# Kernel tuning notes

Hardware: AMD Instinct MI355X
Metric: run time of the kernel (lower is better)

The kernel has to match this reference:

```python
import jax, jax.numpy as jnp
import numpy as np

N = 100_000      # nodes
E = 1_600_000    # edges (avg degree 16)
C_IN, C_H, C_OUT = 32, 64, 64
G = 64           # graphs in batch


def setup_inputs() -> dict:
    key = jax.random.key(0)
    ks = jax.random.split(key, 10)
    x = jax.random.normal(ks[0], (N, C_IN), jnp.float32)
    edge_index = jax.random.randint(ks[1], (2, E), 0, N, dtype=jnp.int64)
    edge_weight = jax.random.uniform(ks[2], (E,), jnp.float32)
    batch = jnp.sort(jax.random.randint(ks[3], (N,), 0, G, dtype=jnp.int64))
    def lin(k, fan_in, fan_out):
        return jax.random.normal(k, (fan_in, fan_out), jnp.float32) / np.float32(np.sqrt(fan_in))
    W1 = lin(ks[4], C_IN, C_H)
    W2 = lin(ks[5], C_H, C_H)
    W3 = lin(ks[6], C_H, C_OUT)
    b1 = jnp.zeros((C_H,), jnp.float32)
    b2 = jnp.zeros((C_H,), jnp.float32)
    b3 = jnp.zeros((C_OUT,), jnp.float32)
    return {"x": x, "edge_weight": edge_weight, "W1": W1, "b1": b1,
            "W2": W2, "b2": b2, "W3": W3, "b3": b3,
            "edge_index": edge_index, "batch": batch}


def _gcn_norm(edge_index, edge_weight, n):
    # PyG GCNConv default: add self-loops (weight 1), symmetric D^-1/2 A D^-1/2 norm.
    loop = jnp.arange(n, dtype=edge_index.dtype)
    src = jnp.concatenate([edge_index[0], loop])
    dst = jnp.concatenate([edge_index[1], loop])
    ew = jnp.concatenate([edge_weight, jnp.ones((n,), edge_weight.dtype)])
    deg = jax.ops.segment_sum(ew, dst, num_segments=n)
    dis = jnp.where(deg > 0, jax.lax.rsqrt(deg), jnp.float32(0))
    norm = dis[src] * ew * dis[dst]
    return src, dst, norm


def _gcn_layer(h, W, b, src, dst, norm, n):
    h = h @ W                                 # [N, out]
    msg = h[src] * norm[:, None]              # gather + scale  [E+N, out]
    agg = jax.ops.segment_sum(msg, dst, num_segments=n)
    return agg + b


def reference(x, edge_weight, W1, b1, W2, b2, W3, b3, edge_index, batch):
    n = x.shape[0]
    src, dst, norm = _gcn_norm(edge_index, edge_weight, n)  # shared across layers
    h = jax.nn.silu(_gcn_layer(x, W1, b1, src, dst, norm, n))
    # Dropout(0.1) is identity in eval mode
    h = jax.nn.silu(_gcn_layer(h, W2, b2, src, dst, norm, n))
    h = jax.nn.silu(_gcn_layer(h, W3, b3, src, dst, norm, n))
    # global_mean_pool over graphs
    sums = jax.ops.segment_sum(h, batch, num_segments=G)
    counts = jax.ops.segment_sum(jnp.ones((n,), h.dtype), batch, num_segments=G)
    return sums / jnp.maximum(counts, 1)[:, None]
```

## Files before the change

kernel.cpp:

```cpp
#include <hip/hip_runtime.h>
#include <hip/hip_fp16.h>
#include <math.h>


#define NB   256
#define PBLK 1024
#define FIXP_SCALE 1048576.0f
#define FIXP_MASK  ((1ULL << 40) - 1)

__device__ __forceinline__ int lower_bound_i(const int* __restrict__ a, int n, int v) {
    int lo = 0, hi = n;
    while (lo < hi) {
        int m = (lo + hi) >> 1;
        if (a[m] < v) lo = m + 1; else hi = m;
    }
    return lo;
}

__global__ __launch_bounds__(256) void k_bhist(const int* __restrict__ dst,
                                               int* __restrict__ hcnt, int e) {
    __shared__ int hist[NB];
    int tid = threadIdx.x, blk = blockIdx.x;
    hist[tid] = 0;
    __syncthreads();
    int chunk = (e + PBLK - 1) / PBLK;
    int lo = blk * chunk, hi = min(e, lo + chunk);
    for (int i = lo + tid; i < hi; i += 256)
        atomicAdd(&hist[dst[i] >> 9], 1);
    __syncthreads();
    hcnt[tid * PBLK + blk] = hist[tid];
}

__global__ __launch_bounds__(256) void k_bscan(int* __restrict__ hcnt,
                                               int* __restrict__ btot) {
    __shared__ int s[256];
    int b = blockIdx.x, tid = threadIdx.x;
    int* row = hcnt + b * PBLK;
    int a0 = row[4 * tid], a1 = row[4 * tid + 1], a2 = row[4 * tid + 2], a3 = row[4 * tid + 3];
    int tsum = a0 + a1 + a2 + a3;
    s[tid] = tsum;
    __syncthreads();
    for (int off = 1; off < 256; off <<= 1) {
        int t = (tid >= off) ? s[tid - off] : 0;
        __syncthreads();
        s[tid] += t;
        __syncthreads();
    }
    int ex = s[tid] - tsum;
    row[4 * tid] = ex;
    row[4 * tid + 1] = ex + a0;
    row[4 * tid + 2] = ex + a0 + a1;
    row[4 * tid + 3] = ex + a0 + a1 + a2;
    if (tid == 255) btot[b] = s[255];
}

__global__ __launch_bounds__(256) void k_bbase(const int* __restrict__ btot,
                                               int* __restrict__ bbase,
                                               int* __restrict__ rowptr, int n, int e) {
    __shared__ int s[256];
    int tid = threadIdx.x;
    int v = btot[tid];
    s[tid] = v;
    __syncthreads();
    for (int off = 1; off < 256; off <<= 1) {
        int t = (tid >= off) ? s[tid - off] : 0;
        __syncthreads();
        s[tid] += t;
        __syncthreads();
    }
    bbase[tid] = s[tid] - v;
    if (tid == 255) bbase[NB] = s[255];
    if (tid == 0) rowptr[n] = e;
}

__global__ __launch_bounds__(256) void k_bpart(const int* __restrict__ src,
                                               const int* __restrict__ dst,
                                               const float* __restrict__ ew,
                                               const int* __restrict__ hcnt,
                                               const int* __restrict__ bbase,
                                               int2* __restrict__ bedge, int e) {
    __shared__ int cur[NB];
    int tid = threadIdx.x, blk = blockIdx.x;
    cur[tid] = bbase[tid] + hcnt[tid * PBLK + blk];
    __syncthreads();
    int chunk = (e + PBLK - 1) / PBLK;
    int lo = blk * chunk, hi = min(e, lo + chunk);
    for (int i = lo + tid; i < hi; i += 256) {
        int d = dst[i];
        int pos = atomicAdd(&cur[d >> 9], 1);
        bedge[pos] = make_int2(src[i] | ((d & 511) << 17), __float_as_int(ew[i]));
    }
}

__global__ __launch_bounds__(256) void k_bucket(const int2* __restrict__ bedge,
                                                const int* __restrict__ bbase,
                                                float* __restrict__ dis,
                                                int* __restrict__ rowptr,
                                                int2* __restrict__ em, int n) {
    __shared__ unsigned long long pk[512];
    __shared__ int cnt[512];
    __shared__ int scn[512];
    __shared__ float sdis[512];
    __shared__ int cur[512];
    int b = blockIdx.x, tid = threadIdx.x;
    int e0 = bbase[b], e1 = bbase[b + 1];
    pk[tid] = 0ULL; pk[tid + 256] = 0ULL;
    __syncthreads();
    for (int i = e0 + tid; i < e1; i += 256) {
        int2 v = bedge[i];
        int dlo = (v.x >> 17) & 511;
        unsigned long long p =
            (1ULL << 40) | (unsigned long long)(__int_as_float(v.y) * FIXP_SCALE);
        atomicAdd(&pk[dlo], p);
    }
    __syncthreads();
#pragma unroll
    for (int k = 0; k < 2; ++k) {
        int i = tid + k * 256;
        unsigned long long v = pk[i];
        int c = (int)(v >> 40);
        cnt[i] = c; scn[i] = c;
        sdis[i] = rsqrtf(1.0f + (float)(v & FIXP_MASK) * (1.0f / FIXP_SCALE));
    }
    __syncthreads();
    for (int off = 1; off < 512; off <<= 1) {
        int i0 = tid, i1 = tid + 256;
        int v0 = (i0 >= off) ? scn[i0 - off] : 0;
        int v1 = (i1 >= off) ? scn[i1 - off] : 0;
        __syncthreads();
        scn[i0] += v0; scn[i1] += v1;
        __syncthreads();
    }
#pragma unroll
    for (int k = 0; k < 2; ++k) {
        int i = tid + k * 256;
        int rb = e0 + scn[i] - cnt[i];
        cur[i] = rb;
        int node = (b << 9) + i;
        if (node < n) { rowptr[node] = rb; dis[node] = sdis[i]; }
    }
    __syncthreads();
    for (int i = e0 + tid; i < e1; i += 256) {
        int2 v = bedge[i];
        int dlo = (v.x >> 17) & 511;
        int pos = atomicAdd(&cur[dlo], 1);
        float w = __int_as_float(v.y) * sdis[dlo];
        em[pos] = make_int2(v.x & 0x1FFFF, __float_as_int(w));
    }
}

__global__ void k_scale(const float* __restrict__ x, const float* __restrict__ dis,
                        __half* __restrict__ hs, int total) {
    int idx = blockIdx.x * blockDim.x + threadIdx.x;
    if (idx < total) hs[idx] = __float2half(x[idx] * dis[idx >> 5]);
}

__device__ __forceinline__ float2 cvt_pair(unsigned int u) {
    __half2 h2 = *(__half2*)&u;
    return __half22float2(h2);
}

template <bool SCALE, typename OUT>
__global__ __launch_bounds__(256, 4) void k_aggmm64(const __half* __restrict__ h,
                                                    const int2* __restrict__ em,
                                                    const int* __restrict__ rowptr,
                                                    const float* __restrict__ dis,
                                                    const float* __restrict__ W,
                                                    const float* __restrict__ bias,
                                                    OUT* __restrict__ out, int n) {
    __shared__ __align__(16) float sacc[4][64];
    __shared__ __align__(8) int2 sme[4][64];
    int lane = threadIdx.x & 63, wv = threadIdx.x >> 6;
    int c = lane & 31, half = lane >> 5;
    const unsigned int* h32 = (const unsigned int*)h;
    float w[64];
#pragma unroll
    for (int k = 0; k < 64; ++k) w[k] = W[k * 64 + lane];
    float bv = bias[lane];
    int wid = (blockIdx.x * blockDim.x + threadIdx.x) >> 6;
    int nw = (gridDim.x * blockDim.x) >> 6;
    for (int node = wid; node < n; node += nw) {
        int lo = rowptr[node], hi = rowptr[node + 1];
        int deg = hi - lo;
        float2 acc = make_float2(0.0f, 0.0f);
        if (half == 0) {
            float2 hv = cvt_pair(h32[(size_t)node * 32 + c]);
            float di = dis[node];
            acc.x = di * hv.x; acc.y = di * hv.y;
        }
        for (int jb = 0; jb < deg; jb += 64) {
            int idx = lo + jb + lane;
            int2 me = (idx < hi) ? em[idx] : make_int2(0, 0);
            sme[wv][lane] = me;
            int rem = deg - jb;
#pragma unroll
            for (int g = 0; g < 4; ++g) {
                if (g * 16 < rem) {
#pragma unroll
                    for (int t = 0; t < 8; ++t) {
                        int2 ev = sme[wv][g * 16 + 2 * t + half];
                        float ww = __int_as_float(ev.y);
                        float2 hf = cvt_pair(h32[(size_t)ev.x * 32 + c]);
                        acc.x = fmaf(ww, hf.x, acc.x);
                        acc.y = fmaf(ww, hf.y, acc.y);
                    }
                }
            }
        }
        acc.x += __shfl_down(acc.x, 32, 64);
        acc.y += __shfl_down(acc.y, 32, 64);
        if (half == 0) ((float2*)sacc[wv])[c] = acc;
        float o = bv;
        const float4* s4 = (const float4*)sacc[wv];
#pragma unroll
        for (int k4 = 0; k4 < 16; ++k4) {
            float4 a4 = s4[k4];
            o = fmaf(a4.x, w[4 * k4 + 0], o);
            o = fmaf(a4.y, w[4 * k4 + 1], o);
            o = fmaf(a4.z, w[4 * k4 + 2], o);
            o = fmaf(a4.w, w[4 * k4 + 3], o);
        }
        o = o / (1.0f + __expf(-o));
        if (SCALE) o *= dis[node];
        if (sizeof(OUT) == 2) {
            ((__half*)out)[(size_t)node * 64 + lane] = __float2half(o);
        } else {
            ((float*)out)[(size_t)node * 64 + lane] = o;
        }
    }
}

__global__ __launch_bounds__(256, 4) void k_aggmm32(const __half* __restrict__ h,
                                                    const int2* __restrict__ em,
                                                    const int* __restrict__ rowptr,
                                                    const float* __restrict__ dis,
                                                    const float* __restrict__ W,
                                                    const float* __restrict__ bias,
                                                    __half* __restrict__ out, int n) {
    __shared__ __align__(16) float sacc[4][32];
    __shared__ __align__(8) int2 sme[4][64];
    int lane = threadIdx.x & 63, wv = threadIdx.x >> 6;
    int c = lane & 15, quarter = lane >> 4;
    const unsigned int* h32 = (const unsigned int*)h;
    float w[32];
#pragma unroll
    for (int k = 0; k < 32; ++k) w[k] = W[k * 64 + lane];
    float bv = bias[lane];
    int wid = (blockIdx.x * blockDim.x + threadIdx.x) >> 6;
    int nw = (gridDim.x * blockDim.x) >> 6;
    for (int node = wid; node < n; node += nw) {
        int lo = rowptr[node], hi = rowptr[node + 1];
        int deg = hi - lo;
        float2 acc = make_float2(0.0f, 0.0f);
        if (quarter == 0) {
            float2 hv = cvt_pair(h32[(size_t)node * 16 + c]);
            float di = dis[node];
            acc.x = di * hv.x; acc.y = di * hv.y;
        }
        for (int jb = 0; jb < deg; jb += 64) {
            int idx = lo + jb + lane;
            int2 me = (idx < hi) ? em[idx] : make_int2(0, 0);
            sme[wv][lane] = me;
            int rem = deg - jb;
#pragma unroll
            for (int g = 0; g < 4; ++g) {
                if (g * 16 < rem) {
#pragma unroll
                    for (int t = 0; t < 4; ++t) {
                        int2 ev = sme[wv][g * 16 + 4 * t + quarter];
                        float ww = __int_as_float(ev.y);
                        float2 hf = cvt_pair(h32[(size_t)ev.x * 16 + c]);
                        acc.x = fmaf(ww, hf.x, acc.x);
                        acc.y = fmaf(ww, hf.y, acc.y);
                    }
                }
            }
        }
        acc.x += __shfl_down(acc.x, 32, 64);
        acc.y += __shfl_down(acc.y, 32, 64);
        acc.x += __shfl_down(acc.x, 16, 64);
        acc.y += __shfl_down(acc.y, 16, 64);
        if (quarter == 0) ((float2*)sacc[wv])[c] = acc;
        float o = bv;
        const float4* s4 = (const float4*)sacc[wv];
#pragma unroll
        for (int k4 = 0; k4 < 8; ++k4) {
            float4 a4 = s4[k4];
            o = fmaf(a4.x, w[4 * k4 + 0], o);
            o = fmaf(a4.y, w[4 * k4 + 1], o);
            o = fmaf(a4.z, w[4 * k4 + 2], o);
            o = fmaf(a4.w, w[4 * k4 + 3], o);
        }
        o = o / (1.0f + __expf(-o));
        o *= dis[node];
        out[(size_t)node * 64 + lane] = __float2half(o);
    }
}

__global__ void k_pool_partial(const float* __restrict__ h, const int* __restrict__ batch,
                               float* __restrict__ acc, int n) {
    int c = threadIdx.x & 63, r = threadIdx.x >> 6;
    int base = blockIdx.x * 128;
    int end = base + 128; if (end > n) end = n;
    float part = 0.0f;
    int cur = -1;
    for (int i = base + r; i < end; i += 4) {
        int g = batch[i];
        if (g != cur) {
            if (cur >= 0) atomicAdd(&acc[cur * 64 + c], part);
            part = 0.0f;
            cur = g;
        }
        part += h[(size_t)i * 64 + c];
    }
    if (cur >= 0) atomicAdd(&acc[cur * 64 + c], part);
}

__global__ void k_pool_final(const float* __restrict__ acc, const int* __restrict__ batch,
                             float* __restrict__ out, int n) {
    int idx = blockIdx.x * blockDim.x + threadIdx.x;
    int g = idx >> 6;
    int lo = lower_bound_i(batch, n, g);
    int hi = lower_bound_i(batch, n, g + 1);
    int cnt = hi - lo;
    out[idx] = acc[idx] / (float)(cnt > 0 ? cnt : 1);
}

extern "C" void kernel_launch(void* const* d_in, const int* in_sizes, int n_in,
                              void* d_out, int out_size, void* d_ws, size_t ws_size,
                              hipStream_t stream) {
    const float* x   = (const float*)d_in[0];
    const float* ew  = (const float*)d_in[1];
    const float* W1  = (const float*)d_in[2];
    const float* b1  = (const float*)d_in[3];
    const float* W2  = (const float*)d_in[4];
    const float* b2  = (const float*)d_in[5];
    const float* W3  = (const float*)d_in[6];
    const float* b3  = (const float*)d_in[7];
    const int*   eidx  = (const int*)d_in[8];
    const int*   batch = (const int*)d_in[9];
    float* out = (float*)d_out;

    const int E = in_sizes[1];
    const int N = in_sizes[9];
    const int G = 64;
    const int* src = eidx;
    const int* dst = eidx + E;

    char* p = (char*)d_ws;
    __half* A     = (__half*)p;                p += (size_t)N * 64 * sizeof(__half);
    __half* B     = (__half*)p;                p += (size_t)N * 64 * sizeof(__half);
    float* C      = (float*)p;                 p += (size_t)N * 64 * sizeof(float);
    float* dis    = (float*)p;                 p += (size_t)N * sizeof(float);
    int*   rowptr = (int*)p;                   p += (size_t)(N + 1) * sizeof(int);
    int*   bbase  = (int*)p;                   p += (size_t)(NB + 1) * sizeof(int);
    float* acc    = (float*)p;                 p += (size_t)G * 64 * sizeof(float);
    p = (char*)(((uintptr_t)p + 7) & ~(uintptr_t)7);
    int2*  em     = (int2*)p;

    int2* bedge = (int2*)A;
    int*  hcnt  = (int*)B;
    int*  btot  = (int*)B + NB * PBLK;

    const int BT = 256;
    const int FUSED_BLOCKS = 3125;

    k_bhist<<<PBLK, 256, 0, stream>>>(dst, hcnt, E);
    k_bscan<<<NB, 256, 0, stream>>>(hcnt, btot);
    k_bbase<<<1, 256, 0, stream>>>(btot, bbase, rowptr, N, E);
    k_bpart<<<PBLK, 256, 0, stream>>>(src, dst, ew, hcnt, bbase, bedge, E);
    k_bucket<<<NB, 256, 0, stream>>>(bedge, bbase, dis, rowptr, em, N);

    k_scale<<<(N * 32 + BT - 1) / BT, BT, 0, stream>>>(x, dis, (__half*)B, N * 32);
    k_aggmm32<<<FUSED_BLOCKS, BT, 0, stream>>>((__half*)B, em, rowptr, dis, W1, b1, A, N);

    k_aggmm64<true, __half><<<FUSED_BLOCKS, BT, 0, stream>>>(A, em, rowptr, dis, W2, b2, B, N);

    k_aggmm64<false, float><<<FUSED_BLOCKS, BT, 0, stream>>>(B, em, rowptr, dis, W3, b3, C, N);

    hipMemsetAsync(acc, 0, (size_t)G * 64 * sizeof(float), stream);
    k_pool_partial<<<(N + 127) / 128, BT, 0, stream>>>(C, batch, acc, N);
    k_pool_final<<<(G * 64) / BT, BT, 0, stream>>>(acc, batch, out, N);
}
```

Baseline: 349.1 us.

## Batch 8 nodes per wave and stream weights instead of holding them in registers

Each wave now aggregates 8 consecutive nodes into shared memory, then runs the dense transform for all 8 at once, loading each weight element from global/cache once per batch rather than keeping the full 64-element weight column in registers. This frees many VGPRs and may raise occupancy and latency hiding for the gather loop. In exchange it re-reads weights from cache per batch and adds shared memory, and contiguous node batching can cause load imbalance or tail waste.

```diff
diff --git a/kernel.cpp b/kernel.cpp
--- a/kernel.cpp
+++ b/kernel.cpp
@@ -160,6 +160,10 @@
     return __half22float2(h2);
 }
 
+__device__ __forceinline__ float silu(float v) {
+    return v / (1.0f + __expf(-v));
+}
+
 template <bool SCALE, typename OUT>
 __global__ __launch_bounds__(256, 4) void k_aggmm64(const __half* __restrict__ h,
                                                     const int2* __restrict__ em,
@@ -168,64 +172,79 @@
                                                     const float* __restrict__ W,
                                                     const float* __restrict__ bias,
                                                     OUT* __restrict__ out, int n) {
-    __shared__ __align__(16) float sacc[4][64];
+    const int NR = 8;
+    __shared__ __align__(16) float sacc[4][NR][64];
     __shared__ __align__(8) int2 sme[4][64];
     int lane = threadIdx.x & 63, wv = threadIdx.x >> 6;
     int c = lane & 31, half = lane >> 5;
     const unsigned int* h32 = (const unsigned int*)h;
-    float w[64];
-#pragma unroll
-    for (int k = 0; k < 64; ++k) w[k] = W[k * 64 + lane];
     float bv = bias[lane];
     int wid = (blockIdx.x * blockDim.x + threadIdx.x) >> 6;
     int nw = (gridDim.x * blockDim.x) >> 6;
-    for (int node = wid; node < n; node += nw) {
-        int lo = rowptr[node], hi = rowptr[node + 1];
-        int deg = hi - lo;
-        float2 acc = make_float2(0.0f, 0.0f);
-        if (half == 0) {
-            float2 hv = cvt_pair(h32[(size_t)node * 32 + c]);
-            float di = dis[node];
-            acc.x = di * hv.x; acc.y = di * hv.y;
-        }
-        for (int jb = 0; jb < deg; jb += 64) {
-            int idx = lo + jb + lane;
-            int2 me = (idx < hi) ? em[idx] : make_int2(0, 0);
-            sme[wv][lane] = me;
-            int rem = deg - jb;
-#pragma unroll
-            for (int g = 0; g < 4; ++g) {
-                if (g * 16 < rem) {
-#pragma unroll
-                    for (int t = 0; t < 8; ++t) {
-                        int2 ev = sme[wv][g * 16 + 2 * t + half];
-                        float ww = __int_as_float(ev.y);
-                        float2 hf = cvt_pair(h32[(size_t)ev.x * 32 + c]);
-                        acc.x = fmaf(ww, hf.x, acc.x);
-                        acc.y = fmaf(ww, hf.y, acc.y);
+    for (int base = wid * NR; base < n; base += nw * NR) {
+#pragma unroll
+        for (int r = 0; r < NR; ++r) {
+            int node = base + r;
+            if (node >= n) break;
+            int lo = rowptr[node], hi = rowptr[node + 1];
+            int deg = hi - lo;
+            float2 acc = make_float2(0.0f, 0.0f);
+            if (half == 0) {
+                float2 hv = cvt_pair(h32[(size_t)node * 32 + c]);
+                float di = dis[node];
+                acc.x = di * hv.x; acc.y = di * hv.y;
+            }
+            for (int jb = 0; jb < deg; jb += 64) {
+                int idx = lo + jb + lane;
+                int2 me = (idx < hi) ? em[idx] : make_int2(0, 0);
+                sme[wv][lane] = me;
+                int rem = deg - jb;
+#pragma unroll
+                for (int g = 0; g < 4; ++g) {
+                    if (g * 16 < rem) {
+#pragma unroll
+                        for (int t = 0; t < 8; ++t) {
+                            int2 ev = sme[wv][g * 16 + 2 * t + half];
+                            float ww = __int_as_float(ev.y);
+                            float2 hf = cvt_pair(h32[(size_t)ev.x * 32 + c]);
+                            acc.x = fmaf(ww, hf.x, acc.x);
+                            acc.y = fmaf(ww, hf.y, acc.y);
+                        }
                     }
                 }
             }
-        }
-        acc.x += __shfl_down(acc.x, 32, 64);
-        acc.y += __shfl_down(acc.y, 32, 64);
-        if (half == 0) ((float2*)sacc[wv])[c] = acc;
-        float o = bv;
-        const float4* s4 = (const float4*)sacc[wv];
-#pragma unroll
+            acc.x += __shfl_down(acc.x, 32, 64);
+            acc.y += __shfl_down(acc.y, 32, 64);
+            if (half == 0) ((float2*)sacc[wv][r])[c] = acc;
+        }
+        float o[NR];
+#pragma unroll
+        for (int r = 0; r < NR; ++r) o[r] = bv;
         for (int k4 = 0; k4 < 16; ++k4) {
-            float4 a4 = s4[k4];
-            o = fmaf(a4.x, w[4 * k4 + 0], o);
-            o = fmaf(a4.y, w[4 * k4 + 1], o);
-            o = fmaf(a4.z, w[4 * k4 + 2], o);
-            o = fmaf(a4.w, w[4 * k4 + 3], o);
-        }
-        o = o / (1.0f + __expf(-o));
-        if (SCALE) o *= dis[node];
-        if (sizeof(OUT) == 2) {
-            ((__half*)out)[(size_t)node * 64 + lane] = __float2half(o);
-        } else {
-            ((float*)out)[(size_t)node * 64 + lane] = o;
+            float w0 = W[(4 * k4 + 0) * 64 + lane];
+            float w1 = W[(4 * k4 + 1) * 64 + lane];
+            float w2 = W[(4 * k4 + 2) * 64 + lane];
+            float w3 = W[(4 * k4 + 3) * 64 + lane];
+#pragma unroll
+            for (int r = 0; r < NR; ++r) {
+                float4 a4 = *(const float4*)&sacc[wv][r][4 * k4];
+                o[r] = fmaf(a4.x, w0, o[r]);
+                o[r] = fmaf(a4.y, w1, o[r]);
+                o[r] = fmaf(a4.z, w2, o[r]);
+                o[r] = fmaf(a4.w, w3, o[r]);
+            }
+        }
+#pragma unroll
+        for (int r = 0; r < NR; ++r) {
+            int node = base + r;
+            if (node >= n) break;
+            float v = silu(o[r]);
+            if (SCALE) v *= dis[node];
+            if (sizeof(OUT) == 2) {
+                ((__half*)out)[(size_t)node * 64 + lane] = __float2half(v);
+            } else {
+                ((float*)out)[(size_t)node * 64 + lane] = v;
+            }
         }
     }
 }
@@ -237,63 +256,77 @@
                                                     const float* __restrict__ W,
                                                     const float* __restrict__ bias,
                                                     __half* __restrict__ out, int n) {
-    __shared__ __align__(16) float sacc[4][32];
+    const int NR = 8;
+    __shared__ __align__(16) float sacc[4][NR][32];
     __shared__ __align__(8) int2 sme[4][64];
     int lane = threadIdx.x & 63, wv = threadIdx.x >> 6;
     int c = lane & 15, quarter = lane >> 4;
     const unsigned int* h32 = (const unsigned int*)h;
-    float w[32];
-#pragma unroll
-    for (int k = 0; k < 32; ++k) w[k] = W[k * 64 + lane];
     float bv = bias[lane];
     int wid = (blockIdx.x * blockDim.x + threadIdx.x) >> 6;
     int nw = (gridDim.x * blockDim.x) >> 6;
-    for (int node = wid; node < n; node += nw) {
-        int lo = rowptr[node], hi = rowptr[node + 1];
-        int deg = hi - lo;
-        float2 acc = make_float2(0.0f, 0.0f);
-        if (quarter == 0) {
-            float2 hv = cvt_pair(h32[(size_t)node * 16 + c]);
-            float di = dis[node];
-            acc.x = di * hv.x; acc.y = di * hv.y;
-        }
-        for (int jb = 0; jb < deg; jb += 64) {
-            int idx = lo + jb + lane;
-            int2 me = (idx < hi) ? em[idx] : make_int2(0, 0);
-            sme[wv][lane] = me;
-            int rem = deg - jb;
-#pragma unroll
-            for (int g = 0; g < 4; ++g) {
-                if (g * 16 < rem) {
-#pragma unroll
-                    for (int t = 0; t < 4; ++t) {
-                        int2 ev = sme[wv][g * 16 + 4 * t + quarter];
-                        float ww = __int_as_float(ev.y);
-                        float2 hf = cvt_pair(h32[(size_t)ev.x * 16 + c]);
-                        acc.x = fmaf(ww, hf.x, acc.x);
-                        acc.y = fmaf(ww, hf.y, acc.y);
+    for (int base = wid * NR; base < n; base += nw * NR) {
+#pragma unroll
+        for (int r = 0; r < NR; ++r) {
+            int node = base + r;
+            if (node >= n) break;
+            int lo = rowptr[node], hi = rowptr[node + 1];
+            int deg = hi - lo;
+            float2 acc = make_float2(0.0f, 0.0f);
+            if (quarter == 0) {
+                float2 hv = cvt_pair(h32[(size_t)node * 16 + c]);
+                float di = dis[node];
+                acc.x = di * hv.x; acc.y = di * hv.y;
+            }
+            for (int jb = 0; jb < deg; jb += 64) {
+                int idx = lo + jb + lane;
+                int2 me = (idx < hi) ? em[idx] : make_int2(0, 0);
+                sme[wv][lane] = me;
+                int rem = deg - jb;
+#pragma unroll
+                for (int g = 0; g < 4; ++g) {
+                    if (g * 16 < rem) {
+#pragma unroll
+                        for (int t = 0; t < 4; ++t) {
+                            int2 ev = sme[wv][g * 16 + 4 * t + quarter];
+                            float ww = __int_as_float(ev.y);
+                            float2 hf = cvt_pair(h32[(size_t)ev.x * 16 + c]);
+                            acc.x = fmaf(ww, hf.x, acc.x);
+                            acc.y = fmaf(ww, hf.y, acc.y);
+                        }
                     }
                 }
             }
-        }
-        acc.x += __shfl_down(acc.x, 32, 64);
-        acc.y += __shfl_down(acc.y, 32, 64);
-        acc.x += __shfl_down(acc.x, 16, 64);
-        acc.y += __shfl_down(acc.y, 16, 64);
-        if (quarter == 0) ((float2*)sacc[wv])[c] = acc;
-        float o = bv;
-        const float4* s4 = (const float4*)sacc[wv];
-#pragma unroll
+            acc.x += __shfl_down(acc.x, 32, 64);
+            acc.y += __shfl_down(acc.y, 32, 64);
+            acc.x += __shfl_down(acc.x, 16, 64);
+            acc.y += __shfl_down(acc.y, 16, 64);
+            if (quarter == 0) ((float2*)sacc[wv][r])[c] = acc;
+        }
+        float o[NR];
+#pragma unroll
+        for (int r = 0; r < NR; ++r) o[r] = bv;
         for (int k4 = 0; k4 < 8; ++k4) {
-            float4 a4 = s4[k4];
-            o = fmaf(a4.x, w[4 * k4 + 0], o);
-            o = fmaf(a4.y, w[4 * k4 + 1], o);
-            o = fmaf(a4.z, w[4 * k4 + 2], o);
-            o = fmaf(a4.w, w[4 * k4 + 3], o);
-        }
-        o = o / (1.0f + __expf(-o));
-        o *= dis[node];
-        out[(size_t)node * 64 + lane] = __float2half(o);
+            float w0 = W[(4 * k4 + 0) * 64 + lane];
+            float w1 = W[(4 * k4 + 1) * 64 + lane];
+            float w2 = W[(4 * k4 + 2) * 64 + lane];
+            float w3 = W[(4 * k4 + 3) * 64 + lane];
+#pragma unroll
+            for (int r = 0; r < NR; ++r) {
+                float4 a4 = *(const float4*)&sacc[wv][r][4 * k4];
+                o[r] = fmaf(a4.x, w0, o[r]);
+                o[r] = fmaf(a4.y, w1, o[r]);
+                o[r] = fmaf(a4.z, w2, o[r]);
+                o[r] = fmaf(a4.w, w3, o[r]);
+            }
+        }
+#pragma unroll
+        for (int r = 0; r < NR; ++r) {
+            int node = base + r;
+            if (node >= n) break;
+            float v = silu(o[r]) * dis[node];
+            out[(size_t)node * 64 + lane] = __float2half(v);
+        }
     }
 }
 
```

After: 365.1 us. +4.6%, slower.
